# Kernel tuning notes

Measured on AMD Instinct MI355X. Metric: run time of the kernel, lower is better.

The kernel has to match this reference:

```python
import jax, jax.numpy as jnp
import numpy as np

B, TC, TD = 256, 200, 50
V_TOK, V_DESC, E, H = 10000, 10000, 300, 512
MARGIN = 0.6


def lstm(x, Wih, Whh, bih, bhh):
    """Unidirectional LSTM over x:(B,T,E) -> all hidden states (B,T,H). PyTorch gate order i,f,g,o."""
    Bb = x.shape[0]
    Hh = Whh.shape[1]
    h0 = jnp.zeros((Bb, Hh), x.dtype)
    c0 = jnp.zeros((Bb, Hh), x.dtype)

    def step(carry, xt):
        h, c = carry
        g = xt @ Wih.T + bih + h @ Whh.T + bhh  # (B,4H)
        i, f, gg, o = jnp.split(g, 4, axis=-1)
        c = jax.nn.sigmoid(f) * c + jax.nn.sigmoid(i) * jnp.tanh(gg)
        h = jax.nn.sigmoid(o) * jnp.tanh(c)
        return (h, c), h

    _, hs = jax.lax.scan(step, (h0, c0), jnp.swapaxes(x, 0, 1))
    return jnp.swapaxes(hs, 0, 1)  # (B,T,H)


def setup_inputs() -> dict:
    ks = jax.random.split(jax.random.key(0), 16)
    s = 0.05
    def p(i, shape):
        return jax.random.normal(ks[i], shape, jnp.float32) * s
    def z(n):
        return jnp.zeros((n,), jnp.float32)
    return {
        'tokens': jax.random.randint(ks[0], (B, TC), 0, V_TOK),
        'tok_len': jax.random.randint(ks[1], (B,), 1, TC + 1),
        'desc_anchor': jax.random.randint(ks[2], (B, TD), 0, V_DESC),
        'desc_anchor_len': jax.random.randint(ks[3], (B,), 1, TD + 1),
        'desc_neg': jax.random.randint(ks[4], (B, TD), 0, V_DESC),
        'desc_neg_len': jax.random.randint(ks[5], (B,), 1, TD + 1),
        'tok_emb': p(6, (V_TOK, E)),
        'tok_Wih': p(7, (4 * H, E)), 'tok_Whh': p(8, (4 * H, H)), 'tok_bih': z(4 * H), 'tok_bhh': z(4 * H),
        'desc_emb': p(9, (V_DESC, E)),
        'desc_Wih': p(10, (4 * H, E)), 'desc_Whh': p(11, (4 * H, H)), 'desc_bih': z(4 * H), 'desc_bhh': z(4 * H),
        'attn_W': p(12, (H, H)), 'attn_b': z(H),
        'attnS_W': p(13, (1, H)), 'attnS_b': z(1),
        'out_W1': p(14, (H, H)), 'out_b1': z(H),
        'out_W2': p(15, (H, H)), 'out_b2': z(H),
    }


def reference(tokens, tok_len, desc_anchor, desc_anchor_len, desc_neg, desc_neg_len,
              tok_emb, tok_Wih, tok_Whh, tok_bih, tok_bhh,
              desc_emb, desc_Wih, desc_Whh, desc_bih, desc_bhh,
              attn_W, attn_b, attnS_W, attnS_b,
              out_W1, out_b1, out_W2, out_b2):
    # ---- code encoding: LSTM + masked self-attention pooling (batched form of the per-sample loop) ----
    feat = jnp.tanh(lstm(tok_emb[tokens], tok_Wih, tok_Whh, tok_bih, tok_bhh))  # (B,TC,H), use_tanh
    scores = (jnp.tanh(feat @ attn_W.T + attn_b) @ attnS_W.T + attnS_b)[..., 0]  # (B,TC)
    mask = jnp.arange(TC)[None, :] < tok_len[:, None]  # valid positions
    w = jax.nn.softmax(jnp.where(mask, scores, -1e9), axis=1)  # softmax over valid tokens only
    pooled = jnp.einsum('bt,bth->bh', w, feat)  # (B,H)
    code_vec = jnp.tanh(jnp.tanh(pooled @ out_W1.T + out_b1) @ out_W2.T + out_b2)

    # ---- desc encoding: final LSTM hidden at true sequence end (pack_padded semantics) ----
    def desc_enc(ids, lens):
        hs = lstm(desc_emb[ids], desc_Wih, desc_Whh, desc_bih, desc_bhh)  # (B,TD,H)
        final = hs[jnp.arange(ids.shape[0]), lens - 1]  # (B,H)
        return jnp.tanh(final)  # use_tanh

    anc = desc_enc(desc_anchor, desc_anchor_len)
    neg = desc_enc(desc_neg, desc_neg_len)

    def cos(a, b):
        denom = jnp.maximum(jnp.linalg.norm(a, axis=-1) * jnp.linalg.norm(b, axis=-1), 1e-8)
        return jnp.sum(a * b, axis=-1) / denom

    loss = jnp.mean(jnp.maximum(MARGIN - cos(code_vec, anc) + cos(code_vec, neg), 1e-6))
    return loss
```

## Files before the change

kernel.cpp:

```cpp
#include <hip/hip_runtime.h>
#include <hip/hip_bf16.h>
#include <math.h>

#define TCc 200
#define TDc 50
#define BATCH 256
#define Ec 300
#define Hc 512
#define VOC 10000
#define EPAD 320
#define KC_E 10
#define KC_H 16

typedef unsigned short u16;
typedef unsigned int u32;
typedef unsigned long long u64;
typedef __bf16 bf16x8 __attribute__((ext_vector_type(8)));
typedef float f32x4 __attribute__((ext_vector_type(4)));

__device__ __forceinline__ float sigf(float x) { return 1.f / (1.f + expf(-x)); }

__device__ __forceinline__ u16 f2bf(float f) {
  unsigned u = __float_as_uint(f);
  unsigned r = (u + 0x7FFFu + ((u >> 16) & 1u)) >> 16;
  return (u16)r;
}
__device__ __forceinline__ float bf2f(u16 v) { return __uint_as_float(((unsigned)v) << 16); }

__device__ __forceinline__ void st_llc(u32* p, u32 v) {
  __hip_atomic_store(p, v, __ATOMIC_RELAXED, __HIP_MEMORY_SCOPE_AGENT);
}
__device__ __forceinline__ u32 ld_llc(const u32* p) {
  return __hip_atomic_load(p, __ATOMIC_RELAXED, __HIP_MEMORY_SCOPE_AGENT);
}
__device__ __forceinline__ u64 ld_llc64(const u64* p) {
  return __hip_atomic_load(p, __ATOMIC_RELAXED, __HIP_MEMORY_SCOPE_AGENT);
}
__device__ __forceinline__ bf16x8 pair_bf16x8(u64 a, u64 b) {
  union { u64 q[2]; bf16x8 v; } t; t.q[0] = a; t.q[1] = b; return t.v;
}

__global__ __launch_bounds__(256) void zero_kernel(float* p, int n) {
  int i = blockIdx.x * 256 + threadIdx.x;
  if (i < n) p[i] = 0.f;
}

__global__ __launch_bounds__(256) void conv_emb_kernel(
    const float* __restrict__ emb, u32* __restrict__ out)
{
  int e = blockIdx.x * 256 + threadIdx.x;
  if (e >= VOC * (EPAD / 2)) return;
  int v = e / (EPAD / 2);
  int k = (e - v * (EPAD / 2)) * 2;
  float a = (k < Ec) ? emb[(size_t)v * Ec + k] : 0.f;
  float b = (k + 1 < Ec) ? emb[(size_t)v * Ec + k + 1] : 0.f;
  out[e] = (u32)f2bf(a) | ((u32)f2bf(b) << 16);
}

template<int GATES>
__global__ __launch_bounds__(256) void conv_wfrag_kernel(
    const float* __restrict__ W, u32* __restrict__ out, int KC, int KREAL, int total)
{
  int e = blockIdx.x * 256 + threadIdx.x;
  if (e >= total) return;
  int jp = e & 3;
  int l = (e >> 2) & 63;
  int si = (e >> 8) & 1;
  int t2 = e >> 9;
  int kc = t2 % KC;
  int nc = t2 / KC;
  int c32 = (si << 4) + (l & 15);
  int srow;
  if (GATES) {
    int ulp = c32 >> 2, g = c32 & 3;
    int unit = ((ulp & 3) << 1) | (ulp >> 2);
    srow = (g << 9) + nc * 8 + unit;
  } else {
    srow = nc * 32 + c32;
  }
  int k = (kc << 5) + ((l >> 4) << 3) + (jp << 1);
  float a = (k < KREAL) ? W[(size_t)srow * KREAL + k] : 0.f;
  float b = (k + 1 < KREAL) ? W[(size_t)srow * KREAL + k + 1] : 0.f;
  out[e] = (u32)f2bf(a) | ((u32)f2bf(b) << 16);
}

__device__ __forceinline__ void bar_signal(u32* cnt, int cg) {
  asm volatile("s_waitcnt vmcnt(0)" ::: "memory");
  __syncthreads();
  if (threadIdx.x == 0)
    __hip_atomic_fetch_add(cnt + ((cg & 7) << 4), 1u,
                           __ATOMIC_RELAXED, __HIP_MEMORY_SCOPE_AGENT);
}
__device__ __forceinline__ void bar_wait(u32* cnt, u32 target) {
  if (threadIdx.x < 8) {
    while (ld_llc(cnt + ((int)threadIdx.x << 4)) < target)
      __builtin_amdgcn_s_sleep(1);
  }
  __syncthreads();
}

struct PArgs {
  const u32* WhhT; const u32* WihT; const u16* embT;
  const u32* WhhD; const u32* WihD; const u16* embD;
  const int* tokens; const int* desc_anchor; const int* desc_neg;
  const int* desc_anchor_len; const int* desc_neg_len;
  const float* tok_bih; const float* tok_bhh;
  const float* desc_bih; const float* desc_bhh;
  u16* hA; u16* hB; u16* hC; u16* hD;
  u16* featB; float* finals;
  u32* flags;
};

template<int ROWS, bool IS_TOK>
__device__ void lstm_phase(
    int lbid, u16* WhF, u16* WiF, float* gsum, int* idsL,
    const u32* __restrict__ WhhF, const u32* __restrict__ WihF, const u16* __restrict__ embB,
    const int* __restrict__ idsA, const int* __restrict__ idsB,
    const int* __restrict__ lenA, const int* __restrict__ lenB,
    const float* __restrict__ bih, const float* __restrict__ bhh,
    u16* __restrict__ h0, u16* __restrict__ h1,
    u16* __restrict__ featB, float* __restrict__ finals,
    u32* cnt, int T)
{
  constexpr int RPW = ROWS / 64;
  const int tid = threadIdx.x;
  const int cg = lbid & 63;
  const int row0 = (lbid >> 6) * ROWS;
  const int w = tid >> 6, l = tid & 63;
  const int rl = tid >> 2, u = tid & 3;
  int gen = 0;

  {
    const uint4* s = (const uint4*)(WhhF + ((size_t)cg << 13));
    uint4* d = (uint4*)WhF;
    #pragma unroll
    for (int i = 0; i < 8; ++i) d[(i << 8) + tid] = s[(i << 8) + tid];
    const uint4* s2 = (const uint4*)(WihF + (size_t)cg * 5120);
    uint4* d2 = (uint4*)WiF;
    #pragma unroll
    for (int i = 0; i < 5; ++i) d2[(i << 8) + tid] = s2[(i << 8) + tid];
  }

  const int ug0 = (cg << 3) + (u << 1);
  float bsv[2][4];
  #pragma unroll
  for (int uu = 0; uu < 2; ++uu)
    #pragma unroll
    for (int g = 0; g < 4; ++g)
      bsv[uu][g] = bih[(g << 9) + ug0 + uu] + bhh[(g << 9) + ug0 + uu];

  const int kcs   = ug0 >> 5;
  const int lanehi = (ug0 >> 3) & 3;
  const int jpos  = ug0 & 7;

  float cc[RPW][2];
  int lens[RPW];
  #pragma unroll
  for (int p = 0; p < RPW; ++p) {
    cc[p][0] = 0.f; cc[p][1] = 0.f;
    int lrow = (p << 6) + rl;
    int row = row0 + lrow;
    lens[p] = IS_TOK ? 0 : ((row < BATCH) ? lenA[row] : lenB[row - BATCH]);
    int rhp = lrow >> 4;
    int lane_s = (rl & 15) | (lanehi << 4);
    size_t off16 = ((((size_t)rhp << 4) + kcs) << 6 | lane_s) << 3 | jpos;
    st_llc((u32*)(h0 + off16), 0u);
  }
  bar_signal(cnt, cg); ++gen;

  for (int t = 0; t < T; ++t) {
    const u16* hin = (t & 1) ? h1 : h0;
    u16* hout = (t & 1) ? h0 : h1;

    if (tid < ROWS) {
      int row = row0 + tid;
      idsL[tid] = IS_TOK ? idsA[row * T + t]
                         : ((row < BATCH) ? idsA[row * T + t] : idsB[(row - BATCH) * T + t]);
    }
    __syncthreads();

    f32x4 acc[RPW][2];
    #pragma unroll
    for (int p = 0; p < RPW; ++p) {
      acc[p][0] = (f32x4){0.f, 0.f, 0.f, 0.f};
      acc[p][1] = (f32x4){0.f, 0.f, 0.f, 0.f};
    }
    const u16* eb[RPW];
    const u64* hfb[RPW];
    #pragma unroll
    for (int p = 0; p < RPW; ++p) {
      int rhp = w + (p << 2);
      int ida = idsL[(rhp << 4) + (l & 15)];
      eb[p] = embB + (size_t)ida * EPAD + ((l >> 4) << 3);
      hfb[p] = (const u64*)hin + ((((size_t)rhp << 4) << 6 | l) << 1);
    }

    #pragma unroll
    for (int kc = 0; kc < KC_E; ++kc) {
      bf16x8 b0 = *(const bf16x8*)(WiF + ((((kc << 1) | 0) << 6 | l) << 3));
      bf16x8 b1 = *(const bf16x8*)(WiF + ((((kc << 1) | 1) << 6 | l) << 3));
      #pragma unroll
      for (int p = 0; p < RPW; ++p) {
        bf16x8 a = *(const bf16x8*)(eb[p] + (kc << 5));
        acc[p][0] = __builtin_amdgcn_mfma_f32_16x16x32_bf16(a, b0, acc[p][0], 0, 0, 0);
        acc[p][1] = __builtin_amdgcn_mfma_f32_16x16x32_bf16(a, b1, acc[p][1], 0, 0, 0);
      }
    }

    bar_wait(cnt, (u32)gen * 8u);

    u64 hw[RPW][2 * KC_H];
    #pragma unroll
    for (int p = 0; p < RPW; ++p)
      #pragma unroll
      for (int kc = 0; kc < KC_H; ++kc) {
        hw[p][2 * kc]     = ld_llc64(hfb[p] + (kc << 7));
        hw[p][2 * kc + 1] = ld_llc64(hfb[p] + (kc << 7) + 1);
      }
    #pragma unroll
    for (int kc = 0; kc < KC_H; ++kc) {
      bf16x8 b0 = *(const bf16x8*)(WhF + ((((kc << 1) | 0) << 6 | l) << 3));
      bf16x8 b1 = *(const bf16x8*)(WhF + ((((kc << 1) | 1) << 6 | l) << 3));
      #pragma unroll
      for (int p = 0; p < RPW; ++p) {
        bf16x8 a = pair_bf16x8(hw[p][2 * kc], hw[p][2 * kc + 1]);
        acc[p][0] = __builtin_amdgcn_mfma_f32_16x16x32_bf16(a, b0, acc[p][0], 0, 0, 0);
        acc[p][1] = __builtin_amdgcn_mfma_f32_16x16x32_bf16(a, b1, acc[p][1], 0, 0, 0);
      }
    }

    float hnv[RPW][2];
    #pragma unroll
    for (int p = 0; p < RPW; ++p) {
      int lr0 = (w << 4) + ((l >> 4) << 2);
      #pragma unroll
      for (int si = 0; si < 2; ++si)
        #pragma unroll
        for (int j = 0; j < 4; ++j)
          gsum[(lr0 + j) * 36 + (si << 4) + (l & 15)] = acc[p][si][j];
      __syncthreads();
      {
        float4 g0 = *(const float4*)&gsum[rl * 36 + (u << 2)];
        float4 g1 = *(const float4*)&gsum[rl * 36 + ((u + 4) << 2)];
        int lrow = (p << 6) + rl;
        int row = row0 + lrow;
        float gi0 = sigf(g0.x + bsv[0][0]);
        float gf0 = sigf(g0.y + bsv[0][1]);
        float gg0 = tanhf(g0.z + bsv[0][2]);
        float go0 = sigf(g0.w + bsv[0][3]);
        float cn0 = gf0 * cc[p][0] + gi0 * gg0;
        cc[p][0] = cn0;
        float hn0 = go0 * tanhf(cn0);
        float gi1 = sigf(g1.x + bsv[1][0]);
        float gf1 = sigf(g1.y + bsv[1][1]);
        float gg1 = tanhf(g1.z + bsv[1][2]);
        float go1 = sigf(g1.w + bsv[1][3]);
        float cn1 = gf1 * cc[p][1] + gi1 * gg1;
        cc[p][1] = cn1;
        float hn1 = go1 * tanhf(cn1);
        hnv[p][0] = hn0; hnv[p][1] = hn1;
        int rhp = lrow >> 4;
        int lane_s = (rl & 15) | (lanehi << 4);
        size_t off16 = ((((size_t)rhp << 4) + kcs) << 6 | lane_s) << 3 | jpos;
        st_llc((u32*)(hout + off16), (u32)f2bf(hn0) | ((u32)f2bf(hn1) << 16));
        if (!IS_TOK) {
          if (t == lens[p] - 1) {
            finals[((size_t)row << 9) + ug0]     = tanhf(hn0);
            finals[((size_t)row << 9) + ug0 + 1] = tanhf(hn1);
          }
        }
      }
      __syncthreads();
    }
    bar_signal(cnt, cg); ++gen;

    if (IS_TOK) {
      #pragma unroll
      for (int p = 0; p < RPW; ++p) {
        int row = row0 + (p << 6) + rl;
        size_t fo = ((size_t)row * TCc + t) << 9;
        *(u32*)(featB + fo + ug0) =
            (u32)f2bf(tanhf(hnv[p][0])) | ((u32)f2bf(tanhf(hnv[p][1])) << 16);
      }
    }
  }
}

__global__ void __launch_bounds__(256, 1) lstm_persist_kernel(PArgs A) {
  __shared__ __align__(16) u16 WhF[KC_H * 2 * 64 * 8];
  __shared__ __align__(16) u16 WiF[KC_E * 2 * 64 * 8];
  __shared__ __align__(16) float gsum[64 * 36];
  __shared__ int idsL[128];
  int bid = blockIdx.x;
  if (bid < 256) {
    u32* cnt = A.flags + ((bid >> 6) << 7);
    size_t hoff = (size_t)(bid >> 6) << 15;
    lstm_phase<64, true>(bid, WhF, WiF, gsum, idsL, A.WhhT, A.WihT, A.embT,
                         A.tokens, nullptr, nullptr, nullptr,
                         A.tok_bih, A.tok_bhh, A.hA + hoff, A.hB + hoff, A.featB, nullptr,
                         cnt, TCc);
  } else {
    int b2 = bid - 256;
    u32* cnt = A.flags + ((4 + (b2 >> 6)) << 7);
    size_t hoff = (size_t)(b2 >> 6) << 16;
    lstm_phase<128, false>(b2, WhF, WiF, gsum, idsL, A.WhhD, A.WihD, A.embD,
                           A.desc_anchor, A.desc_neg, A.desc_anchor_len, A.desc_neg_len,
                           A.desc_bih, A.desc_bhh, A.hC + hoff, A.hD + hoff, nullptr, A.finals,
                           cnt, TDc);
  }
}

__global__ __launch_bounds__(256) void attn_scores_mfma(
    const u16* __restrict__ featB, const u32* __restrict__ WF,
    const float* __restrict__ attn_b, const float* __restrict__ attnS_W,
    const float* __restrict__ attnS_b, float* __restrict__ scores)
{
  __shared__ __align__(16) u16 Af[4 * 16 * 64 * 8];
  const int tid = threadIdx.x;
  const int m0 = blockIdx.x * 64;

  #pragma unroll
  for (int i = 0; i < 16; ++i) {
    int c = (i << 8) + tid;
    int r = c >> 6, kb = c & 63;
    uint4 v = *(const uint4*)(featB + (((size_t)(m0 + r)) << 9) + (kb << 3));
    int kc = kb >> 2, lf = (r & 15) + ((kb & 3) << 4);
    *(uint4*)(Af + ((((r >> 4) * 16 + kc) << 6 | lf) << 3)) = v;
  }
  __syncthreads();

  const int w = tid >> 6, l = tid & 63;
  const u16* WF16 = (const u16*)WF;
  float p[4][4] = {};
  for (int nc = w * 4; nc < w * 4 + 4; ++nc) {
    f32x4 acc[4][2];
    #pragma unroll
    for (int rh = 0; rh < 4; ++rh) {
      acc[rh][0] = (f32x4){0.f, 0.f, 0.f, 0.f};
      acc[rh][1] = (f32x4){0.f, 0.f, 0.f, 0.f};
    }
    #pragma unroll 4
    for (int kc = 0; kc < 16; ++kc) {
      bf16x8 b0 = *(const bf16x8*)(WF16 + ((size_t)((((nc << 4) + kc) << 1 | 0) << 6 | l) << 3));
      bf16x8 b1 = *(const bf16x8*)(WF16 + ((size_t)((((nc << 4) + kc) << 1 | 1) << 6 | l) << 3));
      #pragma unroll
      for (int rh = 0; rh < 4; ++rh) {
        bf16x8 a = *(const bf16x8*)(Af + (((rh * 16 + kc) << 6 | l) << 3));
        acc[rh][0] = __builtin_amdgcn_mfma_f32_16x16x32_bf16(a, b0, acc[rh][0], 0, 0, 0);
        acc[rh][1] = __builtin_amdgcn_mfma_f32_16x16x32_bf16(a, b1, acc[rh][1], 0, 0, 0);
      }
    }
    int c0 = (nc << 5) + (l & 15), c1 = c0 + 16;
    float bb0 = attn_b[c0], sw0 = attnS_W[c0];
    float bb1 = attn_b[c1], sw1 = attnS_W[c1];
    #pragma unroll
    for (int rh = 0; rh < 4; ++rh)
      #pragma unroll
      for (int j = 0; j < 4; ++j)
        p[rh][j] += tanhf(acc[rh][0][j] + bb0) * sw0 + tanhf(acc[rh][1][j] + bb1) * sw1;
  }
  __syncthreads();
  float* red = (float*)Af;
  #pragma unroll
  for (int rh = 0; rh < 4; ++rh)
    #pragma unroll
    for (int j = 0; j < 4; ++j)
      red[(rh * 16 + ((l >> 4) << 2) + j) * 68 + (w << 4) + (l & 15)] = p[rh][j];
  __syncthreads();
  if (tid < 64) {
    float s = attnS_b[0];
    #pragma unroll 8
    for (int q = 0; q < 64; ++q) s += red[tid * 68 + q];
    scores[m0 + tid] = s;
  }
}

__global__ __launch_bounds__(256) void softmax_pool_kernel(
    const float* __restrict__ scores, const int* __restrict__ tok_len,
    const u16* __restrict__ featB, float* __restrict__ pooled)
{
  const int b = blockIdx.x;
  const int tid = threadIdx.x;
  __shared__ float wgt[TCc];
  __shared__ float red[256];
  const int len = tok_len[b];

  float myv = -1e30f;
  if (tid < TCc) {
    float s = scores[b * TCc + tid];
    myv = (tid < len) ? s : -1e9f;
    wgt[tid] = myv;
  }
  red[tid] = myv;
  __syncthreads();
  for (int s = 128; s > 0; s >>= 1) {
    if (tid < s) red[tid] = fmaxf(red[tid], red[tid + s]);
    __syncthreads();
  }
  const float mx = red[0];
  __syncthreads();
  float e = 0.f;
  if (tid < TCc) e = expf(wgt[tid] - mx);
  red[tid] = e;
  __syncthreads();
  for (int s = 128; s > 0; s >>= 1) {
    if (tid < s) red[tid] += red[tid + s];
    __syncthreads();
  }
  const float sum = red[0];
  __syncthreads();
  if (tid < TCc) wgt[tid] = e / sum;
  __syncthreads();

  const u32* featU = (const u32*)featB;
  float a0 = 0.f, a1 = 0.f;
  for (int t = 0; t < TCc; ++t) {
    u32 v = featU[((size_t)b * TCc + t) * 256 + tid];
    float wv = wgt[t];
    a0 = fmaf(wv, bf2f((u16)(v & 0xFFFF)), a0);
    a1 = fmaf(wv, bf2f((u16)(v >> 16)), a1);
  }
  pooled[((size_t)b << 9) + tid * 2] = a0;
  pooled[((size_t)b << 9) + tid * 2 + 1] = a1;
}

__global__ __launch_bounds__(256) void gemm_bias_tanh_kernel(
    const float* __restrict__ A, const float* __restrict__ Bw,
    const float* __restrict__ bias, float* __restrict__ C, int M, int N, int K)
{
  const int r0 = blockIdx.x * 64;
  const int n0 = blockIdx.y * 64;
  const int tid = threadIdx.x;
  const int tu = tid & 15;
  const int tm = tid >> 4;
  __shared__ float As[32][68];
  __shared__ float Bs[32][68];

  float acc[4][4] = {};
  for (int k0 = 0; k0 < K; k0 += 32) {
    #pragma unroll
    for (int i = 0; i < 2; ++i) {
      int lin = tid + (i << 8);
      int kq = lin & 7, m = lin >> 3;
      int k = k0 + (kq << 2);
      int r = r0 + m; if (r >= M) r = M - 1;
      float4 va = *(const float4*)&A[(size_t)r * K + k];
      float4 vb = *(const float4*)&Bw[(size_t)(n0 + m) * K + k];
      As[(kq << 2) + 0][m] = va.x; As[(kq << 2) + 1][m] = va.y;
      As[(kq << 2) + 2][m] = va.z; As[(kq << 2) + 3][m] = va.w;
      Bs[(kq << 2) + 0][m] = vb.x; Bs[(kq << 2) + 1][m] = vb.y;
      Bs[(kq << 2) + 2][m] = vb.z; Bs[(kq << 2) + 3][m] = vb.w;
    }
    __syncthreads();
    #pragma unroll
    for (int kk = 0; kk < 32; ++kk) {
      float4 a = *(const float4*)&As[kk][tm << 2];
      float4 b = *(const float4*)&Bs[kk][tu << 2];
      acc[0][0] = fmaf(a.x, b.x, acc[0][0]); acc[0][1] = fmaf(a.x, b.y, acc[0][1]);
      acc[0][2] = fmaf(a.x, b.z, acc[0][2]); acc[0][3] = fmaf(a.x, b.w, acc[0][3]);
      acc[1][0] = fmaf(a.y, b.x, acc[1][0]); acc[1][1] = fmaf(a.y, b.y, acc[1][1]);
      acc[1][2] = fmaf(a.y, b.z, acc[1][2]); acc[1][3] = fmaf(a.y, b.w, acc[1][3]);
      acc[2][0] = fmaf(a.z, b.x, acc[2][0]); acc[2][1] = fmaf(a.z, b.y, acc[2][1]);
      acc[2][2] = fmaf(a.z, b.z, acc[2][2]); acc[2][3] = fmaf(a.z, b.w, acc[2][3]);
      acc[3][0] = fmaf(a.w, b.x, acc[3][0]); acc[3][1] = fmaf(a.w, b.y, acc[3][1]);
      acc[3][2] = fmaf(a.w, b.z, acc[3][2]); acc[3][3] = fmaf(a.w, b.w, acc[3][3]);
    }
    __syncthreads();
  }
  float bj[4];
  #pragma unroll
  for (int j = 0; j < 4; ++j) bj[j] = bias[n0 + (tu << 2) + j];
  #pragma unroll
  for (int i = 0; i < 4; ++i) {
    int r = r0 + (tm << 2) + i;
    if (r < M) {
      float4 v;
      v.x = tanhf(acc[i][0] + bj[0]); v.y = tanhf(acc[i][1] + bj[1]);
      v.z = tanhf(acc[i][2] + bj[2]); v.w = tanhf(acc[i][3] + bj[3]);
      *(float4*)&C[(size_t)r * N + n0 + (tu << 2)] = v;
    }
  }
}

__global__ __launch_bounds__(256) void loss_kernel(
    const float* __restrict__ code, const float* __restrict__ finals, float* __restrict__ out)
{
  const int b = threadIdx.x;
  const float* cv = code + (size_t)b * Hc;
  const float* av = finals + (size_t)b * Hc;
  const float* nv = finals + (size_t)(BATCH + b) * Hc;
  float dca = 0, dcn = 0, ncc = 0, naa = 0, nnn = 0;
  for (int k = 0; k < Hc; ++k) {
    float c = cv[k], a = av[k], n = nv[k];
    dca = fmaf(c, a, dca);
    dcn = fmaf(c, n, dcn);
    ncc = fmaf(c, c, ncc);
    naa = fmaf(a, a, naa);
    nnn = fmaf(n, n, nnn);
  }
  float cos_a = dca / fmaxf(sqrtf(ncc) * sqrtf(naa), 1e-8f);
  float cos_n = dcn / fmaxf(sqrtf(ncc) * sqrtf(nnn), 1e-8f);
  float hinge = fmaxf(0.6f - cos_a + cos_n, 1e-6f);
  __shared__ float red[256];
  red[b] = hinge;
  __syncthreads();
  for (int s = 128; s > 0; s >>= 1) {
    if (b < s) red[b] += red[b + s];
    __syncthreads();
  }
  if (b == 0) out[0] = red[0] / 256.0f;
}

extern "C" void kernel_launch(void* const* d_in, const int* in_sizes, int n_in,
                              void* d_out, int out_size, void* d_ws, size_t ws_size,
                              hipStream_t stream) {
  const int* tokens          = (const int*)d_in[0];
  const int* tok_len         = (const int*)d_in[1];
  const int* desc_anchor     = (const int*)d_in[2];
  const int* desc_anchor_len = (const int*)d_in[3];
  const int* desc_neg        = (const int*)d_in[4];
  const int* desc_neg_len    = (const int*)d_in[5];
  const float* tok_emb  = (const float*)d_in[6];
  const float* tok_Wih  = (const float*)d_in[7];
  const float* tok_Whh  = (const float*)d_in[8];
  const float* tok_bih  = (const float*)d_in[9];
  const float* tok_bhh  = (const float*)d_in[10];
  const float* desc_emb = (const float*)d_in[11];
  const float* desc_Wih = (const float*)d_in[12];
  const float* desc_Whh = (const float*)d_in[13];
  const float* desc_bih = (const float*)d_in[14];
  const float* desc_bhh = (const float*)d_in[15];
  const float* attn_W   = (const float*)d_in[16];
  const float* attn_b   = (const float*)d_in[17];
  const float* attnS_W  = (const float*)d_in[18];
  const float* attnS_b  = (const float*)d_in[19];
  const float* out_W1   = (const float*)d_in[20];
  const float* out_b1   = (const float*)d_in[21];
  const float* out_W2   = (const float*)d_in[22];
  const float* out_b2   = (const float*)d_in[23];

  float* p = (float*)d_ws;
  size_t off = 0;
  auto alloc = [&](size_t n) { float* q = p + off; off += n; return q; };

  u16*  featB  = (u16*)alloc(13107200);
  u16*  embT   = (u16*)alloc(1600000);
  u16*  embD   = (u16*)alloc(1600000);
  u32*  WihT   = (u32*)alloc(327680);
  u32*  WihD   = (u32*)alloc(327680);
  u32*  WhhT   = (u32*)alloc(524288);
  u32*  WhhD   = (u32*)alloc(524288);
  u32*  attnWF = (u32*)alloc(131072);
  u16*  hA     = (u16*)alloc(65536);
  u16*  hB     = (u16*)alloc(65536);
  u16*  hC     = (u16*)alloc(131072);
  u16*  hD     = (u16*)alloc(131072);
  float* finals = alloc(262144);
  float* scores = alloc(51200);
  float* pooled = alloc(131072);
  float* a2     = alloc(131072);
  float* code   = alloc(131072);
  u32* flags = (u32*)alloc(1024);

  conv_emb_kernel<<<(VOC * (EPAD / 2) + 255) / 256, 256, 0, stream>>>(tok_emb, (u32*)embT);
  conv_emb_kernel<<<(VOC * (EPAD / 2) + 255) / 256, 256, 0, stream>>>(desc_emb, (u32*)embD);
  conv_wfrag_kernel<1><<<2048, 256, 0, stream>>>(tok_Whh, WhhT, KC_H, Hc, 524288);
  conv_wfrag_kernel<1><<<2048, 256, 0, stream>>>(desc_Whh, WhhD, KC_H, Hc, 524288);
  conv_wfrag_kernel<1><<<1280, 256, 0, stream>>>(tok_Wih, WihT, KC_E, Ec, 327680);
  conv_wfrag_kernel<1><<<1280, 256, 0, stream>>>(desc_Wih, WihD, KC_E, Ec, 327680);
  conv_wfrag_kernel<0><<<512, 256, 0, stream>>>(attn_W, attnWF, KC_H, Hc, 131072);
  zero_kernel<<<4, 256, 0, stream>>>((float*)flags, 1024);

  PArgs A;
  A.WhhT = WhhT; A.WihT = WihT; A.embT = embT;
  A.WhhD = WhhD; A.WihD = WihD; A.embD = embD;
  A.tokens = tokens; A.desc_anchor = desc_anchor; A.desc_neg = desc_neg;
  A.desc_anchor_len = desc_anchor_len; A.desc_neg_len = desc_neg_len;
  A.tok_bih = tok_bih; A.tok_bhh = tok_bhh;
  A.desc_bih = desc_bih; A.desc_bhh = desc_bhh;
  A.hA = hA; A.hB = hB; A.hC = hC; A.hD = hD;
  A.featB = featB; A.finals = finals; A.flags = flags;
  lstm_persist_kernel<<<512, 256, 0, stream>>>(A);

  attn_scores_mfma<<<(BATCH * TCc) / 64, 256, 0, stream>>>(
      featB, attnWF, attn_b, attnS_W, attnS_b, scores);
  softmax_pool_kernel<<<BATCH, 256, 0, stream>>>(scores, tok_len, featB, pooled);
  gemm_bias_tanh_kernel<<<dim3(BATCH / 64, Hc / 64), 256, 0, stream>>>(
      pooled, out_W1, out_b1, a2, BATCH, Hc, Hc);
  gemm_bias_tanh_kernel<<<dim3(BATCH / 64, Hc / 64), 256, 0, stream>>>(
      a2, out_W2, out_b2, code, BATCH, Hc, Hc);
  loss_kernel<<<1, 256, 0, stream>>>(code, finals, (float*)d_out);
}
```

Measured before the change: 1.319 ms.

## Bind LSTM row groups to XCDs and use XCD-local L2 for hidden-state exchange

Each block reads its XCC_ID and claims a per-XCD rank, so every row group of the persistent LSTM runs entirely on one XCD. Hidden-state exchange then uses plain cached loads and stores through that XCD's shared L2 instead of agent-scope atomic loads. A 16-deep rotating buffer replaces the ping-pong pair, so a buffer is not reused while stale L1 lines could still hold it. The barrier counters switch to workgroup-scope atomic adds. Correctness now depends on the hardware placing exactly 64 blocks on each XCD, on L1 not serving stale h data, and on workgroup-scope atomics being coherent across CUs, so the risk of hangs or wrong results is significant.

After: 1.183 ms. 10.3% less time.

```diff
diff --git a/kernel.cpp b/kernel.cpp
--- a/kernel.cpp
+++ b/kernel.cpp
@@ -11,6 +11,7 @@
 #define EPAD 320
 #define KC_E 10
 #define KC_H 16
+#define ROT 16
 
 typedef unsigned short u16;
 typedef unsigned int u32;
@@ -27,17 +28,8 @@
 }
 __device__ __forceinline__ float bf2f(u16 v) { return __uint_as_float(((unsigned)v) << 16); }
 
-__device__ __forceinline__ void st_llc(u32* p, u32 v) {
-  __hip_atomic_store(p, v, __ATOMIC_RELAXED, __HIP_MEMORY_SCOPE_AGENT);
-}
-__device__ __forceinline__ u32 ld_llc(const u32* p) {
-  return __hip_atomic_load(p, __ATOMIC_RELAXED, __HIP_MEMORY_SCOPE_AGENT);
-}
-__device__ __forceinline__ u64 ld_llc64(const u64* p) {
-  return __hip_atomic_load(p, __ATOMIC_RELAXED, __HIP_MEMORY_SCOPE_AGENT);
-}
-__device__ __forceinline__ bf16x8 pair_bf16x8(u64 a, u64 b) {
-  union { u64 q[2]; bf16x8 v; } t; t.q[0] = a; t.q[1] = b; return t.v;
+__device__ __forceinline__ u32 l2_add(u32* p, u32 v) {
+  return __hip_atomic_fetch_add(p, v, __ATOMIC_RELAXED, __HIP_MEMORY_SCOPE_WORKGROUP);
 }
 
 __global__ __launch_bounds__(256) void zero_kernel(float* p, int n) {
@@ -87,13 +79,11 @@
 __device__ __forceinline__ void bar_signal(u32* cnt, int cg) {
   asm volatile("s_waitcnt vmcnt(0)" ::: "memory");
   __syncthreads();
-  if (threadIdx.x == 0)
-    __hip_atomic_fetch_add(cnt + ((cg & 7) << 4), 1u,
-                           __ATOMIC_RELAXED, __HIP_MEMORY_SCOPE_AGENT);
+  if (threadIdx.x == 0) l2_add(cnt + ((cg & 7) << 4), 1u);
 }
 __device__ __forceinline__ void bar_wait(u32* cnt, u32 target) {
   if (threadIdx.x < 8) {
-    while (ld_llc(cnt + ((int)threadIdx.x << 4)) < target)
+    while (l2_add(cnt + ((int)threadIdx.x << 4), 0u) < target)
       __builtin_amdgcn_s_sleep(1);
   }
   __syncthreads();
@@ -106,26 +96,26 @@
   const int* desc_anchor_len; const int* desc_neg_len;
   const float* tok_bih; const float* tok_bhh;
   const float* desc_bih; const float* desc_bhh;
-  u16* hA; u16* hB; u16* hC; u16* hD;
+  u16* hTok; u16* hDesc;
   u16* featB; float* finals;
   u32* flags;
 };
 
 template<int ROWS, bool IS_TOK>
 __device__ void lstm_phase(
-    int lbid, u16* WhF, u16* WiF, float* gsum, int* idsL,
+    int cg, int rg, u16* WhF, u16* WiF, float* gsum, int* idsL,
     const u32* __restrict__ WhhF, const u32* __restrict__ WihF, const u16* __restrict__ embB,
     const int* __restrict__ idsA, const int* __restrict__ idsB,
     const int* __restrict__ lenA, const int* __restrict__ lenB,
     const float* __restrict__ bih, const float* __restrict__ bhh,
-    u16* __restrict__ h0, u16* __restrict__ h1,
+    u16* __restrict__ hrot,
     u16* __restrict__ featB, float* __restrict__ finals,
     u32* cnt, int T)
 {
   constexpr int RPW = ROWS / 64;
+  constexpr size_t BUFN = (size_t)ROWS << 9;
   const int tid = threadIdx.x;
-  const int cg = lbid & 63;
-  const int row0 = (lbid >> 6) * ROWS;
+  const int row0 = rg * ROWS;
   const int w = tid >> 6, l = tid & 63;
   const int rl = tid >> 2, u = tid & 3;
   int gen = 0;
@@ -149,9 +139,9 @@
     for (int g = 0; g < 4; ++g)
       bsv[uu][g] = bih[(g << 9) + ug0 + uu] + bhh[(g << 9) + ug0 + uu];
 
-  const int kcs   = ug0 >> 5;
+  const int kcs    = ug0 >> 5;
   const int lanehi = (ug0 >> 3) & 3;
-  const int jpos  = ug0 & 7;
+  const int jpos   = ug0 & 7;
 
   float cc[RPW][2];
   int lens[RPW];
@@ -164,13 +154,13 @@
     int rhp = lrow >> 4;
     int lane_s = (rl & 15) | (lanehi << 4);
     size_t off16 = ((((size_t)rhp << 4) + kcs) << 6 | lane_s) << 3 | jpos;
-    st_llc((u32*)(h0 + off16), 0u);
+    *(u32*)(hrot + off16) = 0u;
   }
   bar_signal(cnt, cg); ++gen;
 
   for (int t = 0; t < T; ++t) {
-    const u16* hin = (t & 1) ? h1 : h0;
-    u16* hout = (t & 1) ? h0 : h1;
+    const u16* hin = hrot + (size_t)(t & (ROT - 1)) * BUFN;
+    u16* hout = hrot + (size_t)((t + 1) & (ROT - 1)) * BUFN;
 
     if (tid < ROWS) {
       int row = row0 + tid;
@@ -186,13 +176,13 @@
       acc[p][1] = (f32x4){0.f, 0.f, 0.f, 0.f};
     }
     const u16* eb[RPW];
-    const u64* hfb[RPW];
+    const u16* hfb[RPW];
     #pragma unroll
     for (int p = 0; p < RPW; ++p) {
       int rhp = w + (p << 2);
       int ida = idsL[(rhp << 4) + (l & 15)];
       eb[p] = embB + (size_t)ida * EPAD + ((l >> 4) << 3);
-      hfb[p] = (const u64*)hin + ((((size_t)rhp << 4) << 6 | l) << 1);
+      hfb[p] = hin + ((((size_t)rhp << 4) << 9) | (l << 3));
     }
 
     #pragma unroll
@@ -209,21 +199,13 @@
 
     bar_wait(cnt, (u32)gen * 8u);
 
-    u64 hw[RPW][2 * KC_H];
-    #pragma unroll
-    for (int p = 0; p < RPW; ++p)
-      #pragma unroll
-      for (int kc = 0; kc < KC_H; ++kc) {
-        hw[p][2 * kc]     = ld_llc64(hfb[p] + (kc << 7));
-        hw[p][2 * kc + 1] = ld_llc64(hfb[p] + (kc << 7) + 1);
-      }
     #pragma unroll
     for (int kc = 0; kc < KC_H; ++kc) {
       bf16x8 b0 = *(const bf16x8*)(WhF + ((((kc << 1) | 0) << 6 | l) << 3));
       bf16x8 b1 = *(const bf16x8*)(WhF + ((((kc << 1) | 1) << 6 | l) << 3));
       #pragma unroll
       for (int p = 0; p < RPW; ++p) {
-        bf16x8 a = pair_bf16x8(hw[p][2 * kc], hw[p][2 * kc + 1]);
+        bf16x8 a = *(const bf16x8*)(hfb[p] + (kc << 9));
         acc[p][0] = __builtin_amdgcn_mfma_f32_16x16x32_bf16(a, b0, acc[p][0], 0, 0, 0);
         acc[p][1] = __builtin_amdgcn_mfma_f32_16x16x32_bf16(a, b1, acc[p][1], 0, 0, 0);
       }
@@ -262,7 +244,7 @@
         int rhp = lrow >> 4;
         int lane_s = (rl & 15) | (lanehi << 4);
         size_t off16 = ((((size_t)rhp << 4) + kcs) << 6 | lane_s) << 3 | jpos;
-        st_llc((u32*)(hout + off16), (u32)f2bf(hn0) | ((u32)f2bf(hn1) << 16));
+        *(u32*)(hout + off16) = (u32)f2bf(hn0) | ((u32)f2bf(hn1) << 16);
         if (!IS_TOK) {
           if (t == lens[p] - 1) {
             finals[((size_t)row << 9) + ug0]     = tanhf(hn0);
@@ -291,21 +273,34 @@
   __shared__ __align__(16) u16 WiF[KC_E * 2 * 64 * 8];
   __shared__ __align__(16) float gsum[64 * 36];
   __shared__ int idsL[128];
-  int bid = blockIdx.x;
-  if (bid < 256) {
-    u32* cnt = A.flags + ((bid >> 6) << 7);
-    size_t hoff = (size_t)(bid >> 6) << 15;
-    lstm_phase<64, true>(bid, WhF, WiF, gsum, idsL, A.WhhT, A.WihT, A.embT,
+  __shared__ int s_claim[2];
+  if (threadIdx.x == 0) {
+    int xcd;
+    asm("s_getreg_b32 %0, hwreg(HW_REG_XCC_ID)" : "=s"(xcd));
+    xcd &= 7;
+    u32 rank = l2_add(A.flags + 1024 + (xcd << 4), 1u);
+    s_claim[0] = xcd;
+    s_claim[1] = (int)rank;
+  }
+  __syncthreads();
+  const int xcd = s_claim[0];
+  const int cg = s_claim[1] & 63;
+
+  if (xcd < 4) {
+    int rg = xcd;
+    u32* cnt = A.flags + (rg << 7);
+    u16* hrot = A.hTok + (size_t)rg * ROT * ((size_t)64 << 9);
+    lstm_phase<64, true>(cg, rg, WhF, WiF, gsum, idsL, A.WhhT, A.WihT, A.embT,
                          A.tokens, nullptr, nullptr, nullptr,
-                         A.tok_bih, A.tok_bhh, A.hA + hoff, A.hB + hoff, A.featB, nullptr,
+                         A.tok_bih, A.tok_bhh, hrot, A.featB, nullptr,
                          cnt, TCc);
   } else {
-    int b2 = bid - 256;
-    u32* cnt = A.flags + ((4 + (b2 >> 6)) << 7);
-    size_t hoff = (size_t)(b2 >> 6) << 16;
-    lstm_phase<128, false>(b2, WhF, WiF, gsum, idsL, A.WhhD, A.WihD, A.embD,
+    int rg = xcd - 4;
+    u32* cnt = A.flags + ((4 + rg) << 7);
+    u16* hrot = A.hDesc + (size_t)rg * ROT * ((size_t)128 << 9);
+    lstm_phase<128, false>(cg, rg, WhF, WiF, gsum, idsL, A.WhhD, A.WihD, A.embD,
                            A.desc_anchor, A.desc_neg, A.desc_anchor_len, A.desc_neg_len,
-                           A.desc_bih, A.desc_bhh, A.hC + hoff, A.hD + hoff, nullptr, A.finals,
+                           A.desc_bih, A.desc_bhh, hrot, nullptr, A.finals,
                            cnt, TDc);
   }
 }
@@ -551,16 +546,14 @@
   u32*  WhhT   = (u32*)alloc(524288);
   u32*  WhhD   = (u32*)alloc(524288);
   u32*  attnWF = (u32*)alloc(131072);
-  u16*  hA     = (u16*)alloc(65536);
-  u16*  hB     = (u16*)alloc(65536);
-  u16*  hC     = (u16*)alloc(131072);
-  u16*  hD     = (u16*)alloc(131072);
+  u16*  hTok   = (u16*)alloc(1048576);
+  u16*  hDesc  = (u16*)alloc(2097152);
   float* finals = alloc(262144);
   float* scores = alloc(51200);
   float* pooled = alloc(131072);
   float* a2     = alloc(131072);
   float* code   = alloc(131072);
-  u32* flags = (u32*)alloc(1024);
+  u32* flags = (u32*)alloc(1280);
 
   conv_emb_kernel<<<(VOC * (EPAD / 2) + 255) / 256, 256, 0, stream>>>(tok_emb, (u32*)embT);
   conv_emb_kernel<<<(VOC * (EPAD / 2) + 255) / 256, 256, 0, stream>>>(desc_emb, (u32*)embD);
@@ -569,7 +562,7 @@
   conv_wfrag_kernel<1><<<1280, 256, 0, stream>>>(tok_Wih, WihT, KC_E, Ec, 327680);
   conv_wfrag_kernel<1><<<1280, 256, 0, stream>>>(desc_Wih, WihD, KC_E, Ec, 327680);
   conv_wfrag_kernel<0><<<512, 256, 0, stream>>>(attn_W, attnWF, KC_H, Hc, 131072);
-  zero_kernel<<<4, 256, 0, stream>>>((float*)flags, 1024);
+  zero_kernel<<<5, 256, 0, stream>>>((float*)flags, 1280);
 
   PArgs A;
   A.WhhT = WhhT; A.WihT = WihT; A.embT = embT;
@@ -578,7 +571,7 @@
   A.desc_anchor_len = desc_anchor_len; A.desc_neg_len = desc_neg_len;
   A.tok_bih = tok_bih; A.tok_bhh = tok_bhh;
   A.desc_bih = desc_bih; A.desc_bhh = desc_bhh;
-  A.hA = hA; A.hB = hB; A.hC = hC; A.hD = hD;
+  A.hTok = hTok; A.hDesc = hDesc;
   A.featB = featB; A.finals = finals; A.flags = flags;
   lstm_persist_kernel<<<512, 256, 0, stream>>>(A);
 
```
